# Kernel tuning notes

Hardware: AMD Instinct MI355X
Metric: run time of the kernel (lower is better)

The kernel has to match this reference:

```python
import jax, jax.numpy as jnp
import numpy as np

N_NODES = 50000


def gcn_conv(x, edge_index, W, b):
    """GCNConv with added self-loops and symmetric D^-1/2 (A+I) D^-1/2 normalization."""
    n = x.shape[0]
    h = x @ W  # [N, out]
    loop = jnp.arange(n, dtype=edge_index.dtype)
    src = jnp.concatenate([edge_index[0], loop])
    dst = jnp.concatenate([edge_index[1], loop])
    ones = jnp.ones(src.shape[0], dtype=x.dtype)
    deg = jax.ops.segment_sum(ones, dst, num_segments=n)  # in-degree incl. self-loop
    dis = jnp.where(deg > 0, jax.lax.rsqrt(deg), 0.0).astype(x.dtype)
    norm = dis[src] * dis[dst]  # [E+N]
    msg = h[src] * norm[:, None]  # gather + scale
    out = jax.ops.segment_sum(msg, dst, num_segments=n)  # scatter-add
    return out + b


def setup_inputs() -> dict:
    key = jax.random.key(0)
    ks = jax.random.split(key, 6)
    d_in, d_h, d_out = 256, 256, 128
    x = jax.random.normal(ks[0], (N_NODES, d_in), dtype=jnp.float32)
    edge_index = jax.random.randint(ks[1], (2, 1600000), 0, N_NODES, dtype=jnp.int64)
    edge_label_index = jax.random.randint(ks[2], (2, 100000), 0, N_NODES, dtype=jnp.int64)
    W1 = jax.random.normal(ks[3], (d_in, d_h), dtype=jnp.float32) * (1.0 / np.sqrt(d_in))
    b1 = jnp.zeros((d_h,), dtype=jnp.float32)
    W2 = jax.random.normal(ks[4], (d_h, d_out), dtype=jnp.float32) * (1.0 / np.sqrt(d_h))
    b2 = jnp.zeros((d_out,), dtype=jnp.float32)
    return {"x": x, "edge_index": edge_index, "edge_label_index": edge_label_index,
            "W1": W1, "b1": b1, "W2": W2, "b2": b2}


def reference(x, edge_index, edge_label_index, W1, b1, W2, b2):
    # encode (eval mode: dropout is identity)
    z = jax.nn.relu(gcn_conv(x, edge_index, W1, b1))
    z = gcn_conv(z, edge_index, W2, b2)  # [N, 128]
    # decode: gather endpoint embeddings and reduce (edge dot-product scores)
    y = jnp.sum(z[edge_label_index[0]] * z[edge_label_index[1]], axis=-1)  # [E_label]
    return y
```

## Files before the change

kernel.cpp:

```cpp
#include <hip/hip_runtime.h>
#include <hip/hip_bf16.h>


#define NPASS 8
#define CAP   96

typedef __attribute__((ext_vector_type(8))) short short8;
typedef __attribute__((ext_vector_type(4))) float f32x4;
typedef __attribute__((ext_vector_type(4))) unsigned int u32x4;

__device__ __forceinline__ unsigned short f2bf_rne(float f) {
  unsigned int b = __float_as_uint(f);
  b += 0x7FFFu + ((b >> 16) & 1u);
  return (unsigned short)(b >> 16);
}
__device__ __forceinline__ float bf_lo(unsigned int u) {
  return __uint_as_float(u << 16);
}
__device__ __forceinline__ float bf_hi(unsigned int u) {
  return __uint_as_float(u & 0xFFFF0000u);
}
__device__ __forceinline__ float i8_0(unsigned int r) { return (float)((int)(r << 24) >> 24); }
__device__ __forceinline__ float i8_1(unsigned int r) { return (float)((int)(r << 16) >> 24); }
__device__ __forceinline__ float i8_2(unsigned int r) { return (float)((int)(r << 8) >> 24); }
__device__ __forceinline__ float i8_3(unsigned int r) { return (float)((int)r >> 24); }

__global__ void prep_k(int* __restrict__ fill, int n,
                       const float* __restrict__ W1, unsigned short* __restrict__ W1t,
                       int K1, int N1, const float* __restrict__ W2,
                       unsigned short* __restrict__ W2t, int K2, int N2) {
  int i = blockIdx.x * blockDim.x + threadIdx.x;
  if (i < n) fill[i] = 0;
  int j = i - n;
  int m1 = K1 * N1;
  if (j >= 0 && j < m1) {
    int k = j / N1, c = j % N1;
    W1t[(size_t)c * K1 + k] = f2bf_rne(W1[j]);
  } else if (j >= m1 && j < m1 + K2 * N2) {
    int j2 = j - m1;
    int k = j2 / N2, c = j2 % N2;
    W2t[(size_t)c * K2 + k] = f2bf_rne(W2[j2]);
  }
}

__global__ void scatter_all_k(const int* __restrict__ src, const int* __restrict__ dst,
                              int* __restrict__ fill, unsigned short* __restrict__ edges,
                              int E, int n) {
  int p = blockIdx.x & (NPASS - 1);
  int c = blockIdx.x >> 3;
  int i = c * 256 + threadIdx.x;
  if (i >= E) return;
  int lo = (int)((long long)n * p / NPASS);
  int hi = (int)((long long)n * (p + 1) / NPASS);
  int d = __builtin_nontemporal_load(&dst[i]);
  if (d < lo || d >= hi) return;
  int s = src[i];
  int slot = atomicAdd(&fill[d], 1);
  if (slot < CAP) edges[(size_t)d * CAP + slot] = (unsigned short)s;
}

__global__ void dis_k(int* __restrict__ fill, float* __restrict__ dis, int n) {
  int i = blockIdx.x * blockDim.x + threadIdx.x;
  if (i < n) {
    int d = fill[i];
    if (d > CAP) { d = CAP; fill[i] = CAP; }
    dis[i] = rsqrtf((float)(d + 1));
  }
}

#define LDST 40
template <bool AF32>
__launch_bounds__(256) __global__
void bfgemm_k(const void* __restrict__ Av,
              const unsigned short* __restrict__ Bt,
              unsigned short* __restrict__ C,
              int M, int N, int K) {
  __shared__ short As[128 * LDST];
  __shared__ short Bs[128 * LDST];
  int t = threadIdx.x;
  int lane = t & 63, wave = t >> 6;
  int quad = lane >> 4, l16 = lane & 15;
  int wm = (wave & 1) * 64, wn = (wave >> 1) * 64;
  int m0 = blockIdx.y * 128, n0 = blockIdx.x * 128;
  f32x4 acc[4][4];
#pragma unroll
  for (int i = 0; i < 4; i++)
#pragma unroll
    for (int j = 0; j < 4; j++) acc[i][j] = (f32x4)0.f;

  for (int k0 = 0; k0 < K; k0 += 32) {
    uint4 av[2], bv[2];
#pragma unroll
    for (int u = 0; u < 2; u++) {
      int idx = t + u * 256;
      int row = idx >> 2, c8 = (idx & 3) * 8;
      int gr = m0 + row;
      if (AF32) {
        const float* A = (const float*)Av;
        float4 f0 = make_float4(0.f, 0.f, 0.f, 0.f), f1 = f0;
        if (gr < M) {
          f0 = *reinterpret_cast<const float4*>(A + (size_t)gr * K + k0 + c8);
          f1 = *reinterpret_cast<const float4*>(A + (size_t)gr * K + k0 + c8 + 4);
        }
        av[u].x = (unsigned)f2bf_rne(f0.x) | ((unsigned)f2bf_rne(f0.y) << 16);
        av[u].y = (unsigned)f2bf_rne(f0.z) | ((unsigned)f2bf_rne(f0.w) << 16);
        av[u].z = (unsigned)f2bf_rne(f1.x) | ((unsigned)f2bf_rne(f1.y) << 16);
        av[u].w = (unsigned)f2bf_rne(f1.z) | ((unsigned)f2bf_rne(f1.w) << 16);
      } else {
        const unsigned short* A = (const unsigned short*)Av;
        av[u] = make_uint4(0u, 0u, 0u, 0u);
        if (gr < M)
          av[u] = *reinterpret_cast<const uint4*>(A + (size_t)gr * K + k0 + c8);
      }
      bv[u] = *reinterpret_cast<const uint4*>(Bt + (size_t)(n0 + row) * K + k0 + c8);
    }
    __syncthreads();
#pragma unroll
    for (int u = 0; u < 2; u++) {
      int idx = t + u * 256;
      int row = idx >> 2, c8 = (idx & 3) * 8;
      *reinterpret_cast<uint4*>(&As[row * LDST + c8]) = av[u];
      *reinterpret_cast<uint4*>(&Bs[row * LDST + c8]) = bv[u];
    }
    __syncthreads();
    short8 af[4], bfr[4];
#pragma unroll
    for (int mt = 0; mt < 4; mt++)
      af[mt] = *reinterpret_cast<const short8*>(&As[(wm + mt * 16 + l16) * LDST + quad * 8]);
#pragma unroll
    for (int nt = 0; nt < 4; nt++)
      bfr[nt] = *reinterpret_cast<const short8*>(&Bs[(wn + nt * 16 + l16) * LDST + quad * 8]);
#pragma unroll
    for (int mt = 0; mt < 4; mt++)
#pragma unroll
      for (int nt = 0; nt < 4; nt++)
        acc[mt][nt] = __builtin_amdgcn_mfma_f32_16x16x32_bf16(af[mt], bfr[nt], acc[mt][nt], 0, 0, 0);
  }
#pragma unroll
  for (int mt = 0; mt < 4; mt++) {
#pragma unroll
    for (int r = 0; r < 4; r++) {
      int grow = m0 + wm + mt * 16 + quad * 4 + r;
      if (grow >= M) continue;
      unsigned short* cp = C + (size_t)grow * N + n0 + wn + l16;
#pragma unroll
      for (int nt = 0; nt < 4; nt++) cp[nt * 16] = f2bf_rne(acc[mt][nt][r]);
    }
  }
}

template <int DIM>
__launch_bounds__(256) __global__
void quant_k(const unsigned short* __restrict__ h, const float* __restrict__ dis,
             void* __restrict__ qv, float* __restrict__ ws, int n) {
  const int C = DIM / 64;
  int wave = threadIdx.x >> 6, lane = threadIdx.x & 63;
  int node = blockIdx.x * 4 + wave;
  if (node >= n) return;
  float v[4];
  if (DIM == 256) {
    uint2 r = *reinterpret_cast<const uint2*>(h + (size_t)node * DIM + lane * 4);
    v[0] = bf_lo(r.x); v[1] = bf_hi(r.x); v[2] = bf_lo(r.y); v[3] = bf_hi(r.y);
  } else {
    unsigned int r = *reinterpret_cast<const unsigned int*>(h + (size_t)node * DIM + lane * 2);
    v[0] = bf_lo(r); v[1] = bf_hi(r);
  }
  float amax = 0.f;
#pragma unroll
  for (int i = 0; i < C; i++) amax = fmaxf(amax, fabsf(v[i]));
#pragma unroll
  for (int off = 32; off; off >>= 1) amax = fmaxf(amax, __shfl_xor(amax, off));
  float inv = amax > 0.f ? 127.f / amax : 0.f;
  int q[4];
#pragma unroll
  for (int i = 0; i < C; i++) {
    int t = (int)rintf(v[i] * inv);
    q[i] = t > 127 ? 127 : (t < -127 ? -127 : t);
  }
  if (DIM == 256) {
    unsigned int p = (unsigned int)(q[0] & 255) | ((unsigned int)(q[1] & 255) << 8) |
                     ((unsigned int)(q[2] & 255) << 16) | ((unsigned int)(q[3] & 255) << 24);
    ((unsigned int*)qv)[(size_t)node * 64 + lane] = p;
  } else {
    unsigned short p = (unsigned short)((q[0] & 255) | ((q[1] & 255) << 8));
    ((unsigned short*)qv)[(size_t)node * 64 + lane] = p;
  }
  if (lane == 0) ws[node] = dis[node] * amax * (1.f / 127.f);
}

template <int VEC, bool RELU, bool OBF>
__launch_bounds__(256) __global__
void aggregate_k(const void* __restrict__ qv, const int* __restrict__ cnt,
                 const unsigned short* __restrict__ edges, const float* __restrict__ ws,
                 const float* __restrict__ dis, const float* __restrict__ bias,
                 void* __restrict__ outv, int n) {
  const int DIM = VEC * 64;
  int wave = threadIdx.x >> 6, lane = threadIdx.x & 63;
  int node = blockIdx.x * (blockDim.x >> 6) + wave;
  if (node >= n) return;
  int start = node * CAP, end = start + cnt[node];
  float di = dis[node];
  const unsigned int* q4 = (const unsigned int*)qv;
  const unsigned short* q2 = (const unsigned short*)qv;
  float acc[VEC];
  {
    float w = ws[node];
    if (VEC == 4) {
      unsigned int r = q4[(size_t)node * 64 + lane];
      acc[0] = i8_0(r) * w; acc[1] = i8_1(r) * w;
      acc[2] = i8_2(r) * w; acc[3] = i8_3(r) * w;
    } else {
      unsigned int r = q2[(size_t)node * 64 + lane];
      acc[0] = i8_0(r) * w; acc[1] = i8_1(r) * w;
    }
  }
  int e = start;
  for (; e + 8 <= end; e += 8) {
    u32x4 ev = __builtin_nontemporal_load(reinterpret_cast<const u32x4*>(&edges[e]));
    unsigned int s[8];
    s[0] = ev.x & 0xFFFFu; s[1] = ev.x >> 16;
    s[2] = ev.y & 0xFFFFu; s[3] = ev.y >> 16;
    s[4] = ev.z & 0xFFFFu; s[5] = ev.z >> 16;
    s[6] = ev.w & 0xFFFFu; s[7] = ev.w >> 16;
    float w[8];
#pragma unroll
    for (int j = 0; j < 8; j++) w[j] = ws[s[j]];
    if (VEC == 4) {
      unsigned int r[8];
#pragma unroll
      for (int j = 0; j < 8; j++) r[j] = q4[(size_t)s[j] * 64 + lane];
#pragma unroll
      for (int j = 0; j < 8; j++) {
        acc[0] = fmaf(i8_0(r[j]), w[j], acc[0]);
        acc[1] = fmaf(i8_1(r[j]), w[j], acc[1]);
        acc[2] = fmaf(i8_2(r[j]), w[j], acc[2]);
        acc[3] = fmaf(i8_3(r[j]), w[j], acc[3]);
      }
    } else {
      unsigned int r[8];
#pragma unroll
      for (int j = 0; j < 8; j++) r[j] = q2[(size_t)s[j] * 64 + lane];
#pragma unroll
      for (int j = 0; j < 8; j++) {
        acc[0] = fmaf(i8_0(r[j]), w[j], acc[0]);
        acc[1] = fmaf(i8_1(r[j]), w[j], acc[1]);
      }
    }
  }
  for (; e < end; e++) {
    unsigned int s = edges[e];
    float w = ws[s];
    if (VEC == 4) {
      unsigned int r = q4[(size_t)s * 64 + lane];
      acc[0] = fmaf(i8_0(r), w, acc[0]);
      acc[1] = fmaf(i8_1(r), w, acc[1]);
      acc[2] = fmaf(i8_2(r), w, acc[2]);
      acc[3] = fmaf(i8_3(r), w, acc[3]);
    } else {
      unsigned int r = q2[(size_t)s * 64 + lane];
      acc[0] = fmaf(i8_0(r), w, acc[0]);
      acc[1] = fmaf(i8_1(r), w, acc[1]);
    }
  }
#pragma unroll
  for (int v = 0; v < VEC; v++) {
    float r = fmaf(di, acc[v], bias[lane * VEC + v]);
    if (RELU) r = fmaxf(r, 0.f);
    acc[v] = r;
  }
  if (OBF) {
    unsigned short* op = (unsigned short*)outv + (size_t)node * DIM + lane * VEC;
    if (VEC == 4) {
      unsigned int p0 = (unsigned int)f2bf_rne(acc[0]) | ((unsigned int)f2bf_rne(acc[1]) << 16);
      unsigned int p1 = (unsigned int)f2bf_rne(acc[2]) | ((unsigned int)f2bf_rne(acc[3]) << 16);
      *reinterpret_cast<uint2*>(op) = make_uint2(p0, p1);
    } else {
      unsigned int p0 = (unsigned int)f2bf_rne(acc[0]) | ((unsigned int)f2bf_rne(acc[1]) << 16);
      *reinterpret_cast<unsigned int*>(op) = p0;
    }
  } else {
    float* op = (float*)outv + (size_t)node * DIM + lane * VEC;
#pragma unroll
    for (int v = 0; v < VEC; v++) op[v] = acc[v];
  }
}

__launch_bounds__(256) __global__
void decode_k(const float* __restrict__ z, const int* __restrict__ ea,
              const int* __restrict__ eb, float* __restrict__ y, int E) {
  int wave = threadIdx.x >> 6, lane = threadIdx.x & 63;
  int e = blockIdx.x * (blockDim.x >> 6) + wave;
  if (e >= E) return;
  int a = ea[e], b = eb[e];
  const float2* za = reinterpret_cast<const float2*>(z + (size_t)a * 128);
  const float2* zb = reinterpret_cast<const float2*>(z + (size_t)b * 128);
  float2 pa = za[lane], pb = zb[lane];
  float s = pa.x * pb.x + pa.y * pb.y;
#pragma unroll
  for (int off = 32; off; off >>= 1) s += __shfl_down(s, off);
  if (lane == 0) y[e] = s;
}

extern "C" void kernel_launch(void* const* d_in, const int* in_sizes, int n_in,
                              void* d_out, int out_size, void* d_ws, size_t ws_size,
                              hipStream_t stream) {
  const float* x = (const float*)d_in[0];
  const int* ei = (const int*)d_in[1];
  const int* eli = (const int*)d_in[2];
  const float* W1 = (const float*)d_in[3];
  const float* b1 = (const float*)d_in[4];
  const float* W2 = (const float*)d_in[5];
  const float* b2 = (const float*)d_in[6];
  float* y = (float*)d_out;

  const int DIN = 256, DH = 256, DOUT = 128;
  const int n = in_sizes[0] / DIN;
  const int E = in_sizes[1] / 2;
  const int EL = in_sizes[2] / 2;
  const int* src = ei;
  const int* dst = ei + E;
  const int* ea = eli;
  const int* eb = eli + EL;

  size_t off = 0;
  auto alloc = [&](size_t bytes) {
    void* p = (char*)d_ws + off;
    off += (bytes + 255) & ~(size_t)255;
    return p;
  };
  int* fill = (int*)alloc((size_t)n * 4);
  float* dis = (float*)alloc((size_t)n * 4);
  float* ws = (float*)alloc((size_t)n * 4);
  unsigned short* edges = (unsigned short*)alloc((size_t)n * CAP * 2);
  unsigned short* W1t = (unsigned short*)alloc((size_t)DIN * DH * 2);
  unsigned short* W2t = (unsigned short*)alloc((size_t)DH * DOUT * 2);
  unsigned short* h1 = (unsigned short*)alloc((size_t)n * DH * 2);
  unsigned short* z1b = (unsigned short*)alloc((size_t)n * DH * 2);
  unsigned int* qbuf = (unsigned int*)alloc((size_t)n * 64 * 4);
  float* z2 = (float*)h1;
  (void)ws_size;

  {
    int total = n + DIN * DH + DH * DOUT;
    prep_k<<<(total + 255) / 256, 256, 0, stream>>>(fill, n, W1, W1t, DIN, DH, W2, W2t, DH, DOUT);
  }

  {
    int EB = (E + 255) / 256;
    scatter_all_k<<<EB * NPASS, 256, 0, stream>>>(src, dst, fill, edges, E, n);
  }
  dis_k<<<(n + 255) / 256, 256, 0, stream>>>(fill, dis, n);

  {
    dim3 grid(DH / 128, (n + 127) / 128);
    bfgemm_k<true><<<grid, 256, 0, stream>>>(x, W1t, h1, n, DH, DIN);
  }
  quant_k<256><<<(n + 3) / 4, 256, 0, stream>>>(h1, dis, qbuf, ws, n);
  aggregate_k<4, true, true><<<(n + 3) / 4, 256, 0, stream>>>(qbuf, fill, edges, ws, dis, b1, z1b, n);

  unsigned short* h2 = h1;
  {
    dim3 grid(DOUT / 128, (n + 127) / 128);
    bfgemm_k<false><<<grid, 256, 0, stream>>>(z1b, W2t, h2, n, DOUT, DH);
  }
  quant_k<128><<<(n + 3) / 4, 256, 0, stream>>>(h2, dis, qbuf, ws, n);
  aggregate_k<2, false, false><<<(n + 3) / 4, 256, 0, stream>>>(qbuf, fill, edges, ws, dis, b2, z2, n);

  decode_k<<<(EL + 3) / 4, 256, 0, stream>>>(z2, ea, eb, y, EL);
}
```

Baseline: 401.8 us.

## Fuse first GEMM and edge scatter into one heterogeneous kernel launch

Merges the layer-1 bf16 GEMM and the CSR-style edge scatter into a single kernel whose block index picks the role, so the compute-bound GEMM blocks run alongside the atomic-bound scatter blocks. The aim is to overlap the two independent stages and save one launch. The cost is that every block now reserves the GEMM's shared memory, which can lower how many lightweight scatter blocks fit per CU. The GEMM block count is padded to a multiple of 8 so the scatter blocks keep their pass alignment.

Measured after the change: 435.2 us. +8.3%, slower.

```diff
diff --git a/kernel.cpp b/kernel.cpp
--- a/kernel.cpp
+++ b/kernel.cpp
@@ -43,22 +43,6 @@
   }
 }
 
-__global__ void scatter_all_k(const int* __restrict__ src, const int* __restrict__ dst,
-                              int* __restrict__ fill, unsigned short* __restrict__ edges,
-                              int E, int n) {
-  int p = blockIdx.x & (NPASS - 1);
-  int c = blockIdx.x >> 3;
-  int i = c * 256 + threadIdx.x;
-  if (i >= E) return;
-  int lo = (int)((long long)n * p / NPASS);
-  int hi = (int)((long long)n * (p + 1) / NPASS);
-  int d = __builtin_nontemporal_load(&dst[i]);
-  if (d < lo || d >= hi) return;
-  int s = src[i];
-  int slot = atomicAdd(&fill[d], 1);
-  if (slot < CAP) edges[(size_t)d * CAP + slot] = (unsigned short)s;
-}
-
 __global__ void dis_k(int* __restrict__ fill, float* __restrict__ dis, int n) {
   int i = blockIdx.x * blockDim.x + threadIdx.x;
   if (i < n) {
@@ -70,18 +54,16 @@
 
 #define LDST 40
 template <bool AF32>
-__launch_bounds__(256) __global__
-void bfgemm_k(const void* __restrict__ Av,
-              const unsigned short* __restrict__ Bt,
-              unsigned short* __restrict__ C,
-              int M, int N, int K) {
-  __shared__ short As[128 * LDST];
-  __shared__ short Bs[128 * LDST];
+__device__ __forceinline__ void gemm_body(const void* __restrict__ Av,
+                                          const unsigned short* __restrict__ Bt,
+                                          unsigned short* __restrict__ C,
+                                          int M, int N, int K, int bx, int by,
+                                          short* As, short* Bs) {
   int t = threadIdx.x;
   int lane = t & 63, wave = t >> 6;
   int quad = lane >> 4, l16 = lane & 15;
   int wm = (wave & 1) * 64, wn = (wave >> 1) * 64;
-  int m0 = blockIdx.y * 128, n0 = blockIdx.x * 128;
+  int m0 = by * 128, n0 = bx * 128;
   f32x4 acc[4][4];
 #pragma unroll
   for (int i = 0; i < 4; i++)
@@ -149,6 +131,42 @@
   }
 }
 
+__launch_bounds__(256) __global__
+void fat1_k(const float* __restrict__ x, const unsigned short* __restrict__ W1t,
+            unsigned short* __restrict__ h1, int M, int N, int K, int NG, int NGreal,
+            const int* __restrict__ src, const int* __restrict__ dst,
+            int* __restrict__ fill, unsigned short* __restrict__ edges, int E, int n) {
+  __shared__ short As[128 * LDST];
+  __shared__ short Bs[128 * LDST];
+  int bid = blockIdx.x;
+  if (bid < NG) {
+    if (bid >= NGreal) return;
+    int nx = N >> 7;
+    gemm_body<true>(x, W1t, h1, M, N, K, bid % nx, bid / nx, As, Bs);
+    return;
+  }
+  int sb = bid - NG;
+  int p = sb & (NPASS - 1);
+  int c = sb >> 3;
+  int i = c * 256 + threadIdx.x;
+  if (i >= E) return;
+  int lo = (int)((long long)n * p / NPASS);
+  int hi = (int)((long long)n * (p + 1) / NPASS);
+  int d = __builtin_nontemporal_load(&dst[i]);
+  if (d < lo || d >= hi) return;
+  int s = src[i];
+  int slot = atomicAdd(&fill[d], 1);
+  if (slot < CAP) edges[(size_t)d * CAP + slot] = (unsigned short)s;
+}
+
+__launch_bounds__(256) __global__
+void bfgemm_k(const unsigned short* __restrict__ A, const unsigned short* __restrict__ Bt,
+              unsigned short* __restrict__ C, int M, int N, int K) {
+  __shared__ short As[128 * LDST];
+  __shared__ short Bs[128 * LDST];
+  gemm_body<false>(A, Bt, C, M, N, K, blockIdx.x, blockIdx.y, As, Bs);
+}
+
 template <int DIM>
 __launch_bounds__(256) __global__
 void quant_k(const unsigned short* __restrict__ h, const float* __restrict__ dis,
@@ -347,21 +365,20 @@
 
   {
     int EB = (E + 255) / 256;
-    scatter_all_k<<<EB * NPASS, 256, 0, stream>>>(src, dst, fill, edges, E, n);
+    int ngreal = (DH / 128) * ((n + 127) / 128);
+    int ng = (ngreal + 7) & ~7;
+    fat1_k<<<ng + EB * NPASS, 256, 0, stream>>>(x, W1t, h1, n, DH, DIN, ng, ngreal,
+                                                src, dst, fill, edges, E, n);
   }
   dis_k<<<(n + 255) / 256, 256, 0, stream>>>(fill, dis, n);
 
-  {
-    dim3 grid(DH / 128, (n + 127) / 128);
-    bfgemm_k<true><<<grid, 256, 0, stream>>>(x, W1t, h1, n, DH, DIN);
-  }
   quant_k<256><<<(n + 3) / 4, 256, 0, stream>>>(h1, dis, qbuf, ws, n);
   aggregate_k<4, true, true><<<(n + 3) / 4, 256, 0, stream>>>(qbuf, fill, edges, ws, dis, b1, z1b, n);
 
   unsigned short* h2 = h1;
   {
     dim3 grid(DOUT / 128, (n + 127) / 128);
-    bfgemm_k<false><<<grid, 256, 0, stream>>>(z1b, W2t, h2, n, DOUT, DH);
+    bfgemm_k<<<grid, 256, 0, stream>>>(z1b, W2t, h2, n, DOUT, DH);
   }
   quant_k<128><<<(n + 3) / 4, 256, 0, stream>>>(h2, dis, qbuf, ws, n);
   aggregate_k<2, false, false><<<(n + 3) / 4, 256, 0, stream>>>(qbuf, fill, edges, ws, dis, b2, z2, n);
```

## Partition edges into destination buckets before scatter to avoid repeated edge scans

Applied to the files above, without the earlier changes.

Replaces the NPASS-fold scan of all edges (each pass reading dst and filtering by range) with a single partition pass that packs (dst offset, src) into 32-bit records grouped per destination range via shared-memory staging and global atomic bucket offsets. A second kernel then scatters each bucket's records into the per-node adjacency lists, keeping the destination-range locality for the fill atomics. This removes the reads of the edge array repeated once per pass, at the cost of an extra intermediate buffer write and read and a 16-bit packing that assumes node ids fit in 16 bits per range.

Measured after the change: 473.7 us. 17.9% more time.

```diff
diff --git a/kernel.cpp b/kernel.cpp
--- a/kernel.cpp
+++ b/kernel.cpp
@@ -25,12 +25,13 @@
 __device__ __forceinline__ float i8_2(unsigned int r) { return (float)((int)(r << 8) >> 24); }
 __device__ __forceinline__ float i8_3(unsigned int r) { return (float)((int)r >> 24); }
 
-__global__ void prep_k(int* __restrict__ fill, int n,
+__global__ void prep_k(int* __restrict__ fill, int* __restrict__ gcnt, int n,
                        const float* __restrict__ W1, unsigned short* __restrict__ W1t,
                        int K1, int N1, const float* __restrict__ W2,
                        unsigned short* __restrict__ W2t, int K2, int N2) {
   int i = blockIdx.x * blockDim.x + threadIdx.x;
   if (i < n) fill[i] = 0;
+  if (i < NPASS) gcnt[i] = 0;
   int j = i - n;
   int m1 = K1 * N1;
   if (j >= 0 && j < m1) {
@@ -43,20 +44,55 @@
   }
 }
 
-__global__ void scatter_all_k(const int* __restrict__ src, const int* __restrict__ dst,
-                              int* __restrict__ fill, unsigned short* __restrict__ edges,
-                              int E, int n) {
-  int p = blockIdx.x & (NPASS - 1);
+__global__ void partition_k(const int* __restrict__ src, const int* __restrict__ dst,
+                            unsigned int* __restrict__ buckets, int* __restrict__ gcnt,
+                            int BCAP, int E, int n) {
+  __shared__ unsigned int rl[NPASS][256];
+  __shared__ int cnt[NPASS], base[NPASS];
+  int t = threadIdx.x;
+  if (t < NPASS) cnt[t] = 0;
+  __syncthreads();
+  int i = blockIdx.x * 256 + t;
+  if (i < E) {
+    int d = __builtin_nontemporal_load(&dst[i]);
+    int s = __builtin_nontemporal_load(&src[i]);
+    int w = (int)((long long)d * NPASS / n);
+    int lo = (int)((long long)n * w / NPASS);
+    unsigned int rec = ((unsigned int)(d - lo) << 16) | (unsigned int)s;
+    int slot = atomicAdd(&cnt[w], 1);
+    rl[w][slot] = rec;
+  }
+  __syncthreads();
+  if (t < NPASS) base[t] = atomicAdd(&gcnt[t], cnt[t]);
+  __syncthreads();
+#pragma unroll
+  for (int b = 0; b < NPASS; b++) {
+    int c = cnt[b], ba = base[b];
+    unsigned int* out = buckets + (size_t)b * BCAP;
+    for (int j = t; j < c; j += 256) {
+      int pos = ba + j;
+      if (pos < BCAP) out[pos] = rl[b][j];
+    }
+  }
+}
+
+__global__ void scatter2_k(const unsigned int* __restrict__ buckets,
+                           const int* __restrict__ gcnt, int BCAP,
+                           int* __restrict__ fill, unsigned short* __restrict__ edges,
+                           int n, int nbw) {
+  int w = blockIdx.x & (NPASS - 1);
   int c = blockIdx.x >> 3;
-  int i = c * 256 + threadIdx.x;
-  if (i >= E) return;
-  int lo = (int)((long long)n * p / NPASS);
-  int hi = (int)((long long)n * (p + 1) / NPASS);
-  int d = __builtin_nontemporal_load(&dst[i]);
-  if (d < lo || d >= hi) return;
-  int s = src[i];
-  int slot = atomicAdd(&fill[d], 1);
-  if (slot < CAP) edges[(size_t)d * CAP + slot] = (unsigned short)s;
+  int cnt = gcnt[w];
+  if (cnt > BCAP) cnt = BCAP;
+  int lo = (int)((long long)n * w / NPASS);
+  const unsigned int* bp = buckets + (size_t)w * BCAP;
+  for (int i = c * 256 + threadIdx.x; i < cnt; i += nbw * 256) {
+    unsigned int rec = __builtin_nontemporal_load(&bp[i]);
+    int d = (int)(rec >> 16) + lo;
+    int s = (int)(rec & 0xFFFFu);
+    int slot = atomicAdd(&fill[d], 1);
+    if (slot < CAP) edges[(size_t)d * CAP + slot] = (unsigned short)s;
+  }
 }
 
 __global__ void dis_k(int* __restrict__ fill, float* __restrict__ dis, int n) {
@@ -329,9 +365,12 @@
     return p;
   };
   int* fill = (int*)alloc((size_t)n * 4);
+  int* gcnt = (int*)alloc((size_t)NPASS * 4);
   float* dis = (float*)alloc((size_t)n * 4);
   float* ws = (float*)alloc((size_t)n * 4);
   unsigned short* edges = (unsigned short*)alloc((size_t)n * CAP * 2);
+  const int BCAP = E / NPASS + 16384;
+  unsigned int* buckets = (unsigned int*)alloc((size_t)NPASS * BCAP * 4);
   unsigned short* W1t = (unsigned short*)alloc((size_t)DIN * DH * 2);
   unsigned short* W2t = (unsigned short*)alloc((size_t)DH * DOUT * 2);
   unsigned short* h1 = (unsigned short*)alloc((size_t)n * DH * 2);
@@ -342,12 +381,14 @@
 
   {
     int total = n + DIN * DH + DH * DOUT;
-    prep_k<<<(total + 255) / 256, 256, 0, stream>>>(fill, n, W1, W1t, DIN, DH, W2, W2t, DH, DOUT);
-  }
-
+    prep_k<<<(total + 255) / 256, 256, 0, stream>>>(fill, gcnt, n, W1, W1t, DIN, DH,
+                                                    W2, W2t, DH, DOUT);
+  }
+
+  partition_k<<<(E + 255) / 256, 256, 0, stream>>>(src, dst, buckets, gcnt, BCAP, E, n);
   {
-    int EB = (E + 255) / 256;
-    scatter_all_k<<<EB * NPASS, 256, 0, stream>>>(src, dst, fill, edges, E, n);
+    const int NBW = 800;
+    scatter2_k<<<NBW * NPASS, 256, 0, stream>>>(buckets, gcnt, BCAP, fill, edges, n, NBW);
   }
   dis_k<<<(n + 255) / 256, 256, 0, stream>>>(fill, dis, n);
 
```

## Replace padded atomic edge bucketing with two-level counting sort into CSR

Applied to the files above, without the earlier changes.

Replaces the 8-pass atomic scatter into fixed 96-slot per-node edge lists with a chunked histogram, prefix scans, a coarse bucket scatter and a per-bucket local sort that together build a compact CSR (row start plus count). Edge data becomes contiguous without padding, and the per-node degree cap is removed. The aggregation kernels now take row offsets and get a scalar prologue that handles unaligned row starts before the 8-wide vector loads. This trades repeated passes over dst and global atomics for several extra small launches, including serial single-thread scans.

After: 398.2 us. No clear change (-0.9%).

```diff
diff --git a/kernel.cpp b/kernel.cpp
--- a/kernel.cpp
+++ b/kernel.cpp
@@ -2,8 +2,7 @@
 #include <hip/hip_bf16.h>
 
 
-#define NPASS 8
-#define CAP   96
+#define CH 4096
 
 typedef __attribute__((ext_vector_type(8))) short short8;
 typedef __attribute__((ext_vector_type(4))) float f32x4;
@@ -25,47 +24,112 @@
 __device__ __forceinline__ float i8_2(unsigned int r) { return (float)((int)(r << 8) >> 24); }
 __device__ __forceinline__ float i8_3(unsigned int r) { return (float)((int)r >> 24); }
 
-__global__ void prep_k(int* __restrict__ fill, int n,
-                       const float* __restrict__ W1, unsigned short* __restrict__ W1t,
+__global__ void prep_k(const float* __restrict__ W1, unsigned short* __restrict__ W1t,
                        int K1, int N1, const float* __restrict__ W2,
                        unsigned short* __restrict__ W2t, int K2, int N2) {
   int i = blockIdx.x * blockDim.x + threadIdx.x;
-  if (i < n) fill[i] = 0;
-  int j = i - n;
   int m1 = K1 * N1;
-  if (j >= 0 && j < m1) {
-    int k = j / N1, c = j % N1;
-    W1t[(size_t)c * K1 + k] = f2bf_rne(W1[j]);
-  } else if (j >= m1 && j < m1 + K2 * N2) {
-    int j2 = j - m1;
+  if (i < m1) {
+    int k = i / N1, c = i % N1;
+    W1t[(size_t)c * K1 + k] = f2bf_rne(W1[i]);
+  } else if (i < m1 + K2 * N2) {
+    int j2 = i - m1;
     int k = j2 / N2, c = j2 % N2;
     W2t[(size_t)c * K2 + k] = f2bf_rne(W2[j2]);
   }
 }
 
-__global__ void scatter_all_k(const int* __restrict__ src, const int* __restrict__ dst,
-                              int* __restrict__ fill, unsigned short* __restrict__ edges,
-                              int E, int n) {
-  int p = blockIdx.x & (NPASS - 1);
-  int c = blockIdx.x >> 3;
-  int i = c * 256 + threadIdx.x;
-  if (i >= E) return;
-  int lo = (int)((long long)n * p / NPASS);
-  int hi = (int)((long long)n * (p + 1) / NPASS);
-  int d = __builtin_nontemporal_load(&dst[i]);
-  if (d < lo || d >= hi) return;
-  int s = src[i];
-  int slot = atomicAdd(&fill[d], 1);
-  if (slot < CAP) edges[(size_t)d * CAP + slot] = (unsigned short)s;
-}
-
-__global__ void dis_k(int* __restrict__ fill, float* __restrict__ dis, int n) {
+__launch_bounds__(256) __global__
+void hist_k(const int* __restrict__ dst, int* __restrict__ cnt, int E, int NB) {
+  __shared__ int h[256];
+  int t = threadIdx.x, b = blockIdx.x;
+  h[t] = 0;
+  __syncthreads();
+  int i0 = b * CH, i1 = i0 + CH;
+  if (i1 > E) i1 = E;
+  for (int i = i0 + t; i < i1; i += 256) {
+    int d = __builtin_nontemporal_load(&dst[i]);
+    atomicAdd(&h[d >> 8], 1);
+  }
+  __syncthreads();
+  cnt[(size_t)t * NB + b] = h[t];
+}
+
+__launch_bounds__(256) __global__
+void scan1_k(int* __restrict__ cnt, int* __restrict__ tot, int NB) {
+  __shared__ int v[1024];
+  int t = threadIdx.x, b = blockIdx.x;
+  for (int j = t; j < NB; j += 256) v[j] = cnt[(size_t)b * NB + j];
+  __syncthreads();
+  if (t == 0) {
+    int s = 0;
+    for (int j = 0; j < NB; j++) { int c = v[j]; v[j] = s; s += c; }
+    tot[b] = s;
+  }
+  __syncthreads();
+  for (int j = t; j < NB; j += 256) cnt[(size_t)b * NB + j] = v[j];
+}
+
+__global__ void scan2_k(const int* __restrict__ tot, int* __restrict__ bstart) {
+  if (threadIdx.x == 0 && blockIdx.x == 0) {
+    int s = 0;
+    for (int b = 0; b < 256; b++) { bstart[b] = s; s += tot[b]; }
+  }
+}
+
+__launch_bounds__(256) __global__
+void scat_k(const int* __restrict__ src, const int* __restrict__ dst,
+            const int* __restrict__ cnt, const int* __restrict__ bstart,
+            unsigned int* __restrict__ rec, int E, int NB) {
+  __shared__ int ofs[256];
+  __shared__ int c2[256];
+  int t = threadIdx.x, b = blockIdx.x;
+  ofs[t] = bstart[t] + cnt[(size_t)t * NB + b];
+  c2[t] = 0;
+  __syncthreads();
+  int i0 = b * CH, i1 = i0 + CH;
+  if (i1 > E) i1 = E;
+  for (int i = i0 + t; i < i1; i += 256) {
+    int d = __builtin_nontemporal_load(&dst[i]);
+    int s = __builtin_nontemporal_load(&src[i]);
+    int bk = d >> 8;
+    int r = atomicAdd(&c2[bk], 1);
+    rec[(size_t)(ofs[bk] + r)] = ((unsigned int)(d & 255) << 16) | (unsigned int)s;
+  }
+}
+
+__launch_bounds__(256) __global__
+void sort2_k(const unsigned int* __restrict__ rec, const int* __restrict__ tot,
+             const int* __restrict__ bstart, unsigned short* __restrict__ edges,
+             int* __restrict__ rowst, int* __restrict__ fill, int n) {
+  __shared__ int hist[256], scanv[256], c2[256];
+  int t = threadIdx.x, b = blockIdx.x;
+  int nrec = tot[b], bs = bstart[b];
+  hist[t] = 0;
+  __syncthreads();
+  const unsigned int* rp = rec + bs;
+  for (int i = t; i < nrec; i += 256) atomicAdd(&hist[rp[i] >> 16], 1);
+  __syncthreads();
+  if (t == 0) {
+    int s = 0;
+    for (int k = 0; k < 256; k++) { scanv[k] = s; s += hist[k]; }
+  }
+  __syncthreads();
+  int d = b * 256 + t;
+  if (d < n) { fill[d] = hist[t]; rowst[d] = bs + scanv[t]; }
+  c2[t] = 0;
+  __syncthreads();
+  for (int i = t; i < nrec; i += 256) {
+    unsigned int r = rp[i];
+    int dl = (int)(r >> 16);
+    int pos = scanv[dl] + atomicAdd(&c2[dl], 1);
+    edges[(size_t)bs + pos] = (unsigned short)r;
+  }
+}
+
+__global__ void dis_k(const int* __restrict__ fill, float* __restrict__ dis, int n) {
   int i = blockIdx.x * blockDim.x + threadIdx.x;
-  if (i < n) {
-    int d = fill[i];
-    if (d > CAP) { d = CAP; fill[i] = CAP; }
-    dis[i] = rsqrtf((float)(d + 1));
-  }
+  if (i < n) dis[i] = rsqrtf((float)(fill[i] + 1));
 }
 
 #define LDST 40
@@ -190,15 +254,15 @@
 
 template <int VEC, bool RELU, bool OBF>
 __launch_bounds__(256) __global__
-void aggregate_k(const void* __restrict__ qv, const int* __restrict__ cnt,
-                 const unsigned short* __restrict__ edges, const float* __restrict__ ws,
-                 const float* __restrict__ dis, const float* __restrict__ bias,
-                 void* __restrict__ outv, int n) {
+void aggregate_k(const void* __restrict__ qv, const int* __restrict__ fill,
+                 const int* __restrict__ rowst, const unsigned short* __restrict__ edges,
+                 const float* __restrict__ ws, const float* __restrict__ dis,
+                 const float* __restrict__ bias, void* __restrict__ outv, int n) {
   const int DIM = VEC * 64;
   int wave = threadIdx.x >> 6, lane = threadIdx.x & 63;
   int node = blockIdx.x * (blockDim.x >> 6) + wave;
   if (node >= n) return;
-  int start = node * CAP, end = start + cnt[node];
+  int start = rowst[node], end = start + fill[node];
   float di = dis[node];
   const unsigned int* q4 = (const unsigned int*)qv;
   const unsigned short* q2 = (const unsigned short*)qv;
@@ -215,6 +279,21 @@
     }
   }
   int e = start;
+  for (; e < end && (e & 7); e++) {
+    unsigned int s = edges[e];
+    float w = ws[s];
+    if (VEC == 4) {
+      unsigned int r = q4[(size_t)s * 64 + lane];
+      acc[0] = fmaf(i8_0(r), w, acc[0]);
+      acc[1] = fmaf(i8_1(r), w, acc[1]);
+      acc[2] = fmaf(i8_2(r), w, acc[2]);
+      acc[3] = fmaf(i8_3(r), w, acc[3]);
+    } else {
+      unsigned int r = q2[(size_t)s * 64 + lane];
+      acc[0] = fmaf(i8_0(r), w, acc[0]);
+      acc[1] = fmaf(i8_1(r), w, acc[1]);
+    }
+  }
   for (; e + 8 <= end; e += 8) {
     u32x4 ev = __builtin_nontemporal_load(reinterpret_cast<const u32x4*>(&edges[e]));
     unsigned int s[8];
@@ -322,6 +401,9 @@
   const int* ea = eli;
   const int* eb = eli + EL;
 
+  const int NB = (E + CH - 1) / CH;
+  const int NBUCK = (n + 255) / 256;
+
   size_t off = 0;
   auto alloc = [&](size_t bytes) {
     void* p = (char*)d_ws + off;
@@ -329,9 +411,14 @@
     return p;
   };
   int* fill = (int*)alloc((size_t)n * 4);
+  int* rowst = (int*)alloc((size_t)n * 4);
+  int* cnt = (int*)alloc((size_t)256 * NB * 4);
+  int* tot = (int*)alloc((size_t)256 * 4);
+  int* bstart = (int*)alloc((size_t)256 * 4);
+  unsigned int* rec = (unsigned int*)alloc((size_t)E * 4);
   float* dis = (float*)alloc((size_t)n * 4);
   float* ws = (float*)alloc((size_t)n * 4);
-  unsigned short* edges = (unsigned short*)alloc((size_t)n * CAP * 2);
+  unsigned short* edges = (unsigned short*)alloc((size_t)E * 2);
   unsigned short* W1t = (unsigned short*)alloc((size_t)DIN * DH * 2);
   unsigned short* W2t = (unsigned short*)alloc((size_t)DH * DOUT * 2);
   unsigned short* h1 = (unsigned short*)alloc((size_t)n * DH * 2);
@@ -340,15 +427,14 @@
   float* z2 = (float*)h1;
   (void)ws_size;
 
-  {
-    int total = n + DIN * DH + DH * DOUT;
-    prep_k<<<(total + 255) / 256, 256, 0, stream>>>(fill, n, W1, W1t, DIN, DH, W2, W2t, DH, DOUT);
-  }
-
-  {
-    int EB = (E + 255) / 256;
-    scatter_all_k<<<EB * NPASS, 256, 0, stream>>>(src, dst, fill, edges, E, n);
-  }
+  prep_k<<<(DIN * DH + DH * DOUT + 255) / 256, 256, 0, stream>>>(W1, W1t, DIN, DH,
+                                                                 W2, W2t, DH, DOUT);
+
+  hist_k<<<NB, 256, 0, stream>>>(dst, cnt, E, NB);
+  scan1_k<<<256, 256, 0, stream>>>(cnt, tot, NB);
+  scan2_k<<<1, 64, 0, stream>>>(tot, bstart);
+  scat_k<<<NB, 256, 0, stream>>>(src, dst, cnt, bstart, rec, E, NB);
+  sort2_k<<<NBUCK, 256, 0, stream>>>(rec, tot, bstart, edges, rowst, fill, n);
   dis_k<<<(n + 255) / 256, 256, 0, stream>>>(fill, dis, n);
 
   {
@@ -356,7 +442,8 @@
     bfgemm_k<true><<<grid, 256, 0, stream>>>(x, W1t, h1, n, DH, DIN);
   }
   quant_k<256><<<(n + 3) / 4, 256, 0, stream>>>(h1, dis, qbuf, ws, n);
-  aggregate_k<4, true, true><<<(n + 3) / 4, 256, 0, stream>>>(qbuf, fill, edges, ws, dis, b1, z1b, n);
+  aggregate_k<4, true, true><<<(n + 3) / 4, 256, 0, stream>>>(qbuf, fill, rowst, edges,
+                                                              ws, dis, b1, z1b, n);
 
   unsigned short* h2 = h1;
   {
@@ -364,7 +451,8 @@
     bfgemm_k<false><<<grid, 256, 0, stream>>>(z1b, W2t, h2, n, DOUT, DH);
   }
   quant_k<128><<<(n + 3) / 4, 256, 0, stream>>>(h2, dis, qbuf, ws, n);
-  aggregate_k<2, false, false><<<(n + 3) / 4, 256, 0, stream>>>(qbuf, fill, edges, ws, dis, b2, z2, n);
+  aggregate_k<2, false, false><<<(n + 3) / 4, 256, 0, stream>>>(qbuf, fill, rowst, edges,
+                                                                ws, dis, b2, z2, n);
 
   decode_k<<<(EL + 3) / 4, 256, 0, stream>>>(z2, ea, eb, y, EL);
 }
```
